# Kernel optimization log

Hardware: AMD Instinct MI355X
Metric: run time of the kernel (lower is better)

Reference implementation:

```python
import jax, jax.numpy as jnp
import numpy as np


def setup_inputs() -> dict:
    key = jax.random.key(0)
    k1, k2 = jax.random.split(key)
    lut = jax.random.normal(k1, (1, 3, 33, 33, 33), dtype=jnp.float32)
    x = jax.random.uniform(k2, (8, 3, 1024, 1024), dtype=jnp.float32)
    return {"lut": lut, "x": x}


def reference(lut, x):
    # lut: [1, 3, D, D, D]; x: [B, 3, H, W] in [0,1]
    D = lut.shape[-1]
    lut0 = lut[0]  # [3, D, D, D], broadcast over batch (lut batch == 1)

    v = jnp.clip(x, 0.0, 1.0) * (D - 1)            # [B, 3, H, W]
    v = jnp.transpose(v, (0, 2, 3, 1))             # [B, H, W, 3]
    i0 = jnp.floor(v).astype(jnp.int32)            # [B, H, W, 3]
    i1 = jnp.minimum(i0 + 1, D - 1)
    f = v - i0.astype(v.dtype)                     # fractional part

    r0, g0, b0 = i0[..., 0], i0[..., 1], i0[..., 2]
    r1, g1, b1 = i1[..., 0], i1[..., 1], i1[..., 2]
    fr, fg, fb = f[..., 0], f[..., 1], f[..., 2]

    def gather(rr, gg, bb):
        # lut0[:, rr, gg, bb] -> [3, B, H, W] -> [B, 3, H, W]
        return jnp.transpose(lut0[:, rr, gg, bb], (1, 0, 2, 3))

    c000 = gather(r0, g0, b0)
    c100 = gather(r1, g0, b0)
    c010 = gather(r0, g1, b0)
    c110 = gather(r1, g1, b0)
    c001 = gather(r0, g0, b1)
    c101 = gather(r1, g0, b1)
    c011 = gather(r0, g1, b1)
    c111 = gather(r1, g1, b1)

    one = jnp.float32(1.0)
    w000 = ((one - fr) * (one - fg) * (one - fb))[:, None]
    w100 = (fr * (one - fg) * (one - fb))[:, None]
    w010 = ((one - fr) * fg * (one - fb))[:, None]
    w110 = (fr * fg * (one - fb))[:, None]
    w001 = ((one - fr) * (one - fg) * fb)[:, None]
    w101 = (fr * (one - fg) * fb)[:, None]
    w011 = ((one - fr) * fg * fb)[:, None]
    w111 = (fr * fg * fb)[:, None]

    out = (c000 * w000 + c100 * w100 + c010 * w010 + c110 * w110 +
           c001 * w001 + c101 * w101 + c011 * w011 + c111 * w111)
    return out  # [B, 3, H, W]
```

## Files before the change

kernel.cpp:

```cpp
#include <hip/hip_runtime.h>
#include <hip/hip_fp16.h>


#define D   33
#define D2  (33 * 33)
#define D3  (33 * 33 * 33)
#define NP  (D3 - 1)
#define HW  (1024 * 1024)
#define BATCH 8
#define QHW (HW / 4)
#define NG  (BATCH * QHW)
#define CHUNKS 256
#define GPC (NG / CHUNKS)
#define THREADS 1024
#define NXCD 8
#define CPX (CHUNKS / NXCD)

__global__ __launch_bounds__(THREADS) void lut3d_kernel(
    const float* __restrict__ lut, const float* __restrict__ x,
    float* __restrict__ out)
{
    const int bid = blockIdx.x;
    const int xcd = bid & (NXCD - 1);
    const int s   = bid >> 3;
    const int cl  = s / 3;
    const int c   = s - 3 * cl;
    const int chunk = xcd * CPX + cl;

    __shared__ __half2 ls[NP];
    {
        const float* lc = lut + c * D3;
        for (int i = threadIdx.x; i < NP; i += THREADS) {
            ls[i] = __halves2half2(__float2half_rn(lc[i]),
                                   __float2half_rn(lc[i + 1]));
        }
    }
    __syncthreads();

    const int tid  = threadIdx.x;
    const int base = chunk * GPC;

    #pragma unroll 1
    for (int it = 0; it < GPC / THREADS; ++it) {
        const int g = base + it * THREADS + tid;
        const int b = g >> 18;
        const int p = (g & (QHW - 1)) * 4;

        const float* xb = x + (size_t)b * 3 * HW + p;
        const float4 xr = *(const float4*)(xb);
        const float4 xg = *(const float4*)(xb + HW);
        const float4 xB = *(const float4*)(xb + 2 * HW);

        const float rr[4] = {xr.x, xr.y, xr.z, xr.w};
        const float gg[4] = {xg.x, xg.y, xg.z, xg.w};
        const float bb[4] = {xB.x, xB.y, xB.z, xB.w};
        float oo[4];

        #pragma unroll
        for (int j = 0; j < 4; ++j) {
            const float vr = fminf(fmaxf(rr[j], 0.f) * 32.f, 31.999998f);
            const float vg = fminf(fmaxf(gg[j], 0.f) * 32.f, 31.999998f);
            const float vb = fminf(fmaxf(bb[j], 0.f) * 32.f, 31.999998f);

            const int r0 = (int)vr, g0 = (int)vg, b0 = (int)vb;
            const float fr = vr - (float)r0;
            const float fg = vg - (float)g0;
            const float fb = vb - (float)b0;

            const int idx = __mul24(r0, D2) + __mul24(g0, D) + b0;

            const __half2 h00 = ls[idx];
            const __half2 h01 = ls[idx + D];
            const __half2 h10 = ls[idx + D2];
            const __half2 h11 = ls[idx + D2 + D];

            const float wb0 = 1.0f - fb;
            const float c00 = __low2float(h00) * wb0 + __high2float(h00) * fb;
            const float c01 = __low2float(h01) * wb0 + __high2float(h01) * fb;
            const float c10 = __low2float(h10) * wb0 + __high2float(h10) * fb;
            const float c11 = __low2float(h11) * wb0 + __high2float(h11) * fb;

            const float c0 = c00 + fg * (c01 - c00);
            const float c1 = c10 + fg * (c11 - c10);
            oo[j] = c0 + fr * (c1 - c0);
        }

        float* ob = out + (size_t)b * 3 * HW + (size_t)c * HW + p;
        *(float4*)ob = make_float4(oo[0], oo[1], oo[2], oo[3]);
    }
}

extern "C" void kernel_launch(void* const* d_in, const int* in_sizes, int n_in,
                              void* d_out, int out_size, void* d_ws, size_t ws_size,
                              hipStream_t stream) {
    const float* lut = (const float*)d_in[0];
    const float* x   = (const float*)d_in[1];
    float* out = (float*)d_out;

    dim3 grid(3 * CHUNKS);
    lut3d_kernel<<<grid, THREADS, 0, stream>>>(lut, x, out);
}
```

Before: 221.5 us.

## Use packed fp16 dot2 for b-axis interpolation, nontemporal stores, 2D grid

Replaces the b-axis lerp, which unpacked each half2 to two floats and did two multiplies, with a single v_dot2_f32_f16 against packed fp16 weights. The weights go through round-toward-zero fp16 conversion, which adds a small precision loss. Output writes become nontemporal stores to limit cache pollution. The grid changes from a 1D XCD-swizzled mapping to a plain 2D (channel, chunk) grid, so the three channel blocks of a chunk are now likely to land on different XCDs and lose L2 reuse of x.

Result: no change. 221.2 us (-0.2%).

```diff
diff --git a/kernel.cpp b/kernel.cpp
--- a/kernel.cpp
+++ b/kernel.cpp
@@ -13,26 +13,37 @@
 #define CHUNKS 256
 #define GPC (NG / CHUNKS)
 #define THREADS 1024
-#define NXCD 8
-#define CPX (CHUNKS / NXCD)
+
+typedef __fp16 h16;
+typedef __attribute__((ext_vector_type(2))) __fp16 h16x2;
+typedef __attribute__((ext_vector_type(4))) float f32x4;
+
+#if __has_builtin(__builtin_amdgcn_fdot2)
+#define DOT2(a, b) __builtin_amdgcn_fdot2((a), (b), 0.0f, false)
+#else
+static __device__ __forceinline__ float dot2_asm(h16x2 a, h16x2 b) {
+    float d;
+    asm("v_dot2_f32_f16 %0, %1, %2, 0" : "=v"(d) : "v"(a), "v"(b));
+    return d;
+}
+#define DOT2(a, b) dot2_asm((a), (b))
+#endif
 
 __global__ __launch_bounds__(THREADS) void lut3d_kernel(
     const float* __restrict__ lut, const float* __restrict__ x,
     float* __restrict__ out)
 {
-    const int bid = blockIdx.x;
-    const int xcd = bid & (NXCD - 1);
-    const int s   = bid >> 3;
-    const int cl  = s / 3;
-    const int c   = s - 3 * cl;
-    const int chunk = xcd * CPX + cl;
+    const int c     = blockIdx.x;
+    const int chunk = blockIdx.y;
 
-    __shared__ __half2 ls[NP];
+    __shared__ h16x2 ls[NP];
     {
         const float* lc = lut + c * D3;
         for (int i = threadIdx.x; i < NP; i += THREADS) {
-            ls[i] = __halves2half2(__float2half_rn(lc[i]),
-                                   __float2half_rn(lc[i + 1]));
+            h16x2 v;
+            v.x = (h16)lc[i];
+            v.y = (h16)lc[i + 1];
+            ls[i] = v;
         }
     }
     __syncthreads();
@@ -67,18 +78,18 @@
             const float fg = vg - (float)g0;
             const float fb = vb - (float)b0;
 
-            const int idx = __mul24(r0, D2) + __mul24(g0, D) + b0;
+            const int idx = r0 * D2 + g0 * D + b0;
 
-            const __half2 h00 = ls[idx];
-            const __half2 h01 = ls[idx + D];
-            const __half2 h10 = ls[idx + D2];
-            const __half2 h11 = ls[idx + D2 + D];
+            const h16x2 h00 = ls[idx];
+            const h16x2 h01 = ls[idx + D];
+            const h16x2 h10 = ls[idx + D2];
+            const h16x2 h11 = ls[idx + D2 + D];
 
-            const float wb0 = 1.0f - fb;
-            const float c00 = __low2float(h00) * wb0 + __high2float(h00) * fb;
-            const float c01 = __low2float(h01) * wb0 + __high2float(h01) * fb;
-            const float c10 = __low2float(h10) * wb0 + __high2float(h10) * fb;
-            const float c11 = __low2float(h11) * wb0 + __high2float(h11) * fb;
+            const h16x2 w = __builtin_amdgcn_cvt_pkrtz(1.0f - fb, fb);
+            const float c00 = DOT2(h00, w);
+            const float c01 = DOT2(h01, w);
+            const float c10 = DOT2(h10, w);
+            const float c11 = DOT2(h11, w);
 
             const float c0 = c00 + fg * (c01 - c00);
             const float c1 = c10 + fg * (c11 - c10);
@@ -86,7 +97,9 @@
         }
 
         float* ob = out + (size_t)b * 3 * HW + (size_t)c * HW + p;
-        *(float4*)ob = make_float4(oo[0], oo[1], oo[2], oo[3]);
+        f32x4 ov;
+        ov.x = oo[0]; ov.y = oo[1]; ov.z = oo[2]; ov.w = oo[3];
+        __builtin_nontemporal_store(ov, (f32x4*)ob);
     }
 }
 
@@ -97,6 +110,6 @@
     const float* x   = (const float*)d_in[1];
     float* out = (float*)d_out;
 
-    dim3 grid(3 * CHUNKS);
+    dim3 grid(3, CHUNKS);
     lut3d_kernel<<<grid, THREADS, 0, stream>>>(lut, x, out);
 }
```
